# Performance work log

Measured on AMD Instinct MI355X. Metric: run time of the kernel, lower is better.

## Reference

```python
import jax, jax.numpy as jnp
import numpy as np

LAYER_SIZES = [128, 128, 64, 64, 64, 1]  # sMLP([128,128,64,64,64,1], 'relu')
B, DX, DY = 1024, 64, 64


def setup_inputs() -> dict:
    key = jax.random.key(0)
    ks = jax.random.split(key, 8)
    inp = {
        'x': jax.random.normal(ks[0], (B, DX), dtype=jnp.float32),
        'y': jax.random.normal(ks[1], (B, DY), dtype=jnp.float32),
    }
    dims = [DX + DY] + LAYER_SIZES
    for i in range(len(LAYER_SIZES)):
        fan_in, fan_out = dims[i], dims[i + 1]
        scale = jnp.sqrt(2.0 / (fan_in + fan_out)).astype(jnp.float32)  # glorot-like
        inp[f'W{i}'] = jax.random.normal(ks[2 + i % 6], (fan_in, fan_out), dtype=jnp.float32) * scale
        inp[f'b{i}'] = jnp.zeros((fan_out,), dtype=jnp.float32)
    return inp


def _mlp(h, Ws, bs):
    n = len(Ws)
    for i in range(n):
        h = h @ Ws[i] + bs[i]
        if i < n - 1:  # relu on hidden layers, linear output
            h = jax.nn.relu(h)
    return h


def reference(x, y, W0, b0, W1, b1, W2, b2, W3, b3, W4, b4, W5, b5):
    Bn = x.shape[0]
    dx, dy = x.shape[1], y.shape[1]
    # all-pairs tile+concat: row (i*B + j) = concat(x[j], y[i])
    x_tiled = jnp.broadcast_to(x[None, :, :], (Bn, Bn, dx))
    y_tiled = jnp.broadcast_to(y[:, None, :], (Bn, Bn, dy))
    xy_pairs = jnp.concatenate([x_tiled, y_tiled], axis=2).reshape(Bn * Bn, dx + dy)
    scores = _mlp(xy_pairs, [W0, W1, W2, W3, W4, W5], [b0, b1, b2, b3, b4, b5])
    scores = scores.reshape(Bn, Bn).T  # final[p, q] = g(x[p], y[q])
    return scores
```

## Files before the change

### kernel.cpp

```cpp
#include <hip/hip_runtime.h>

#define NB 1024

typedef _Float16 f16x8 __attribute__((ext_vector_type(8)));
typedef float f32x4 __attribute__((ext_vector_type(4)));

union ABu { uint4 u; f16x8 v; _Float16 h[8]; };

__global__ void prep_ac(const float* __restrict__ x, const float* __restrict__ y,
                        const float* __restrict__ W0, const float* __restrict__ b0,
                        _Float16* __restrict__ Af, _Float16* __restrict__ Cf) {
    __shared__ float row[64];
    int b = blockIdx.x;
    int t = threadIdx.x;
    bool isC = b >= 1024;
    int r = isC ? b - 1024 : b;
    const float* src = isC ? y : x;
    if (t < 64) row[t] = src[r * 64 + t];
    __syncthreads();
    const float* w = W0 + (isC ? 64 * 128 : 0);
    float acc = isC ? b0[t] : 0.f;
#pragma unroll
    for (int k = 0; k < 64; k++) acc += row[k] * w[k * 128 + t];
    (isC ? Cf : Af)[r * 128 + t] = (_Float16)acc;
}

__global__ void prep_img(const float* __restrict__ W1, const float* __restrict__ W2,
                         const float* __restrict__ W3, const float* __restrict__ W4,
                         _Float16* __restrict__ img) {
    int i = blockIdx.x * 256 + threadIdx.x;
    float val;
    if (i < 16384) {
        int j = i & 7, cc = (i >> 3) & 15, gg = (i >> 7) & 3, ks = (i >> 9) & 3, ft = i >> 11;
        int k = 32 * ks + 8 * gg + j, n = 16 * ft + cc;
        val = W1[k * 128 + n];
    } else if (i < 24576) {
        int d = i - 16384;
        int j = d & 7, cc = (d >> 3) & 15, gg = (d >> 7) & 3, ks = (d >> 9) & 3, ft = d >> 11;
        int s = 32 * ks + 8 * gg + j;
        int H = s >> 6, sp = s & 63;
        int a = ((sp >> 5) & 1) | (((sp >> 2) & 1) << 1);
        int gs = (sp >> 3) & 3, rr = sp & 3;
        int fin = 64 * H + 16 * a + 4 * gs + rr, n = 16 * ft + cc;
        val = W2[fin * 64 + n];
    } else {
        int d = (i < 28672) ? i - 24576 : i - 28672;
        const float* W = (i < 28672) ? W3 : W4;
        int j = d & 7, cc = (d >> 3) & 15, gg = (d >> 7) & 3, ks = (d >> 9) & 1, ft = d >> 10;
        int s = 32 * ks + 8 * gg + j;
        int a = ((s >> 5) & 1) | (((s >> 2) & 1) << 1);
        int gs = (s >> 3) & 3, rr = s & 3;
        int fin = 16 * a + 4 * gs + rr, n = 16 * ft + cc;
        val = W[fin * 64 + n];
    }
    img[i] = (_Float16)val;
}

#define MFMA(a, b, d) (d) = __builtin_amdgcn_mfma_f32_16x16x32_f16((a), (b), (d), 0, 0, 0)

#define W2OFF 32768
#define W3OFF 49152
#define W4OFF 57344

__launch_bounds__(512, 4)
__global__ void critic_main(const _Float16* __restrict__ Af, const _Float16* __restrict__ Cf,
                            const _Float16* __restrict__ Wimg,
                            const float* __restrict__ b1, const float* __restrict__ b2,
                            const float* __restrict__ b3, const float* __restrict__ b4,
                            const float* __restrict__ W5, const float* __restrict__ b5,
                            float* __restrict__ out) {
    __shared__ _Float16 Wl[32768];
    int tid = threadIdx.x;

    {
        const uint4* src = (const uint4*)Wimg;
        uint4* dst = (uint4*)Wl;
#pragma unroll
        for (int r = 0; r < 8; r++) dst[r * 512 + tid] = src[r * 512 + tid];
    }
    __syncthreads();

    int w = tid >> 6, lane = tid & 63;
    int g = lane >> 4, c = lane & 15;
    int pw = (blockIdx.x >> 6) * 16 + w * 2;
    int qb = (blockIdx.x & 63) * 16;
    const char* WB = (const char*)Wl;
    int lo = lane * 16;

    ABu af[4][2];
#pragma unroll
    for (int ks = 0; ks < 4; ks++) {
        ABu cv; cv.u = *(const uint4*)&Cf[(qb + c) * 128 + ks * 32 + 8 * g];
#pragma unroll
        for (int pt = 0; pt < 2; pt++) {
            ABu av; av.u = *(const uint4*)&Af[(pw + pt) * 128 + ks * 32 + 8 * g];
            f16x8 s = av.v + cv.v;
            f16x8 z = {};
            af[ks][pt].v = __builtin_elementwise_max(s, z);
        }
    }

    ABu bh1[4][2];
#pragma unroll
    for (int ft = 0; ft < 8; ft++) {
        const int Hq = ft >> 2, a3 = ft & 3, ksp = a3 & 1, hi = a3 >> 1;
        f32x4 binit = *(const f32x4*)&b1[ft * 16 + 4 * g];
        f32x4 acc[2] = {binit, binit};
#pragma unroll
        for (int ks = 0; ks < 4; ks++) {
            ABu wf; wf.u = *(const uint4*)(WB + ft * 4096 + ks * 1024 + lo);
#pragma unroll
            for (int pt = 0; pt < 2; pt++) MFMA(wf.v, af[ks][pt].v, acc[pt]);
        }
#pragma unroll
        for (int pt = 0; pt < 2; pt++)
#pragma unroll
            for (int r = 0; r < 4; r++)
                bh1[Hq * 2 + ksp][pt].h[hi * 4 + r] = (_Float16)fmaxf(acc[pt][r], 0.f);
    }

    ABu bh2[2][2];
#pragma unroll
    for (int ft = 0; ft < 4; ft++) {
        const int ksp = ft & 1, hi = ft >> 1;
        f32x4 binit = *(const f32x4*)&b2[ft * 16 + 4 * g];
        f32x4 acc[2] = {binit, binit};
#pragma unroll
        for (int ks = 0; ks < 4; ks++) {
            ABu wf; wf.u = *(const uint4*)(WB + W2OFF + ft * 4096 + ks * 1024 + lo);
#pragma unroll
            for (int pt = 0; pt < 2; pt++) MFMA(wf.v, bh1[ks][pt].v, acc[pt]);
        }
#pragma unroll
        for (int pt = 0; pt < 2; pt++)
#pragma unroll
            for (int r = 0; r < 4; r++)
                bh2[ksp][pt].h[hi * 4 + r] = (_Float16)fmaxf(acc[pt][r], 0.f);
    }

    ABu bh3[2][2];
#pragma unroll
    for (int ft = 0; ft < 4; ft++) {
        const int ksp = ft & 1, hi = ft >> 1;
        f32x4 binit = *(const f32x4*)&b3[ft * 16 + 4 * g];
        f32x4 acc[2] = {binit, binit};
#pragma unroll
        for (int ks = 0; ks < 2; ks++) {
            ABu wf; wf.u = *(const uint4*)(WB + W3OFF + ft * 2048 + ks * 1024 + lo);
#pragma unroll
            for (int pt = 0; pt < 2; pt++) MFMA(wf.v, bh2[ks][pt].v, acc[pt]);
        }
#pragma unroll
        for (int pt = 0; pt < 2; pt++)
#pragma unroll
            for (int r = 0; r < 4; r++)
                bh3[ksp][pt].h[hi * 4 + r] = (_Float16)fmaxf(acc[pt][r], 0.f);
    }

    float s0 = 0.f, s1 = 0.f;
#pragma unroll
    for (int ft = 0; ft < 4; ft++) {
        f32x4 binit = *(const f32x4*)&b4[ft * 16 + 4 * g];
        f32x4 ww    = *(const f32x4*)&W5[ft * 16 + 4 * g];
        f32x4 acc[2] = {binit, binit};
#pragma unroll
        for (int ks = 0; ks < 2; ks++) {
            ABu wf; wf.u = *(const uint4*)(WB + W4OFF + ft * 2048 + ks * 1024 + lo);
#pragma unroll
            for (int pt = 0; pt < 2; pt++) MFMA(wf.v, bh3[ks][pt].v, acc[pt]);
        }
#pragma unroll
        for (int r = 0; r < 4; r++) {
            s0 += fmaxf(acc[0][r], 0.f) * ww[r];
            s1 += fmaxf(acc[1][r], 0.f) * ww[r];
        }
    }

    float b5s = b5[0];
    s0 += __shfl_xor(s0, 16); s0 += __shfl_xor(s0, 32);
    s1 += __shfl_xor(s1, 16); s1 += __shfl_xor(s1, 32);
    if (lane < 16) {
        out[(pw + 0) * NB + qb + c] = s0 + b5s;
        out[(pw + 1) * NB + qb + c] = s1 + b5s;
    }
}

extern "C" void kernel_launch(void* const* d_in, const int* in_sizes, int n_in,
                              void* d_out, int out_size, void* d_ws, size_t ws_size,
                              hipStream_t stream) {
    const float* x  = (const float*)d_in[0];
    const float* y  = (const float*)d_in[1];
    const float* W0 = (const float*)d_in[2];
    const float* b0 = (const float*)d_in[3];
    const float* W1 = (const float*)d_in[4];
    const float* b1 = (const float*)d_in[5];
    const float* W2 = (const float*)d_in[6];
    const float* b2 = (const float*)d_in[7];
    const float* W3 = (const float*)d_in[8];
    const float* b3 = (const float*)d_in[9];
    const float* W4 = (const float*)d_in[10];
    const float* b4 = (const float*)d_in[11];
    const float* W5 = (const float*)d_in[12];
    const float* b5 = (const float*)d_in[13];
    float* out = (float*)d_out;

    char* ws = (char*)d_ws;
    _Float16* Af   = (_Float16*)ws;
    _Float16* Cf   = (_Float16*)(ws + 262144);
    _Float16* Wimg = (_Float16*)(ws + 524288);

    prep_ac<<<2048, 128, 0, stream>>>(x, y, W0, b0, Af, Cf);
    prep_img<<<128, 256, 0, stream>>>(W1, W2, W3, W4, Wimg);
    critic_main<<<4096, 512, 0, stream>>>(Af, Cf, Wimg,
                                          b1, b2, b3, b4, W5, b5, out);
}
```

Measured before the change: 80.70 us.

## Process four p-rows per wave and pack fp16 conversions with cvt_pkrtz

Each wave now handles four p-rows instead of two. Every weight fragment loaded from LDS therefore feeds four MFMAs instead of two, and the grid halves to 2048 blocks, so the per-block cost of staging the 64KB weight image into LDS is paid half as often. Activation conversion to fp16 now uses packed round-toward-zero conversions, which take fewer instructions but round differently. The larger register footprint forces launch bounds down to 2 blocks per CU, which cuts occupancy.

```diff
diff --git a/kernel.cpp b/kernel.cpp
--- a/kernel.cpp
+++ b/kernel.cpp
@@ -5,7 +5,12 @@
 typedef _Float16 f16x8 __attribute__((ext_vector_type(8)));
 typedef float f32x4 __attribute__((ext_vector_type(4)));
 
-union ABu { uint4 u; f16x8 v; _Float16 h[8]; };
+union ABu { uint4 u; f16x8 v; _Float16 h[8]; unsigned int w[4]; };
+
+__device__ __forceinline__ unsigned int pkrtz(float a, float b) {
+    __fp16 r2 __attribute__((ext_vector_type(2))) = __builtin_amdgcn_cvt_pkrtz(a, b);
+    return __builtin_bit_cast(unsigned int, r2);
+}
 
 __global__ void prep_ac(const float* __restrict__ x, const float* __restrict__ y,
                         const float* __restrict__ W0, const float* __restrict__ b0,
@@ -62,7 +67,7 @@
 #define W3OFF 49152
 #define W4OFF 57344
 
-__launch_bounds__(512, 4)
+__launch_bounds__(512, 2)
 __global__ void critic_main(const _Float16* __restrict__ Af, const _Float16* __restrict__ Cf,
                             const _Float16* __restrict__ Wimg,
                             const float* __restrict__ b1, const float* __restrict__ b2,
@@ -82,17 +87,17 @@
 
     int w = tid >> 6, lane = tid & 63;
     int g = lane >> 4, c = lane & 15;
-    int pw = (blockIdx.x >> 6) * 16 + w * 2;
+    int pw = (blockIdx.x >> 6) * 32 + w * 4;
     int qb = (blockIdx.x & 63) * 16;
     const char* WB = (const char*)Wl;
     int lo = lane * 16;
 
-    ABu af[4][2];
+    ABu af[4][4];
 #pragma unroll
     for (int ks = 0; ks < 4; ks++) {
         ABu cv; cv.u = *(const uint4*)&Cf[(qb + c) * 128 + ks * 32 + 8 * g];
 #pragma unroll
-        for (int pt = 0; pt < 2; pt++) {
+        for (int pt = 0; pt < 4; pt++) {
             ABu av; av.u = *(const uint4*)&Af[(pw + pt) * 128 + ks * 32 + 8 * g];
             f16x8 s = av.v + cv.v;
             f16x8 z = {};
@@ -100,88 +105,100 @@
         }
     }
 
-    ABu bh1[4][2];
+    ABu bh1[4][4];
 #pragma unroll
     for (int ft = 0; ft < 8; ft++) {
         const int Hq = ft >> 2, a3 = ft & 3, ksp = a3 & 1, hi = a3 >> 1;
         f32x4 binit = *(const f32x4*)&b1[ft * 16 + 4 * g];
-        f32x4 acc[2] = {binit, binit};
+        f32x4 acc[4] = {binit, binit, binit, binit};
 #pragma unroll
         for (int ks = 0; ks < 4; ks++) {
             ABu wf; wf.u = *(const uint4*)(WB + ft * 4096 + ks * 1024 + lo);
 #pragma unroll
-            for (int pt = 0; pt < 2; pt++) MFMA(wf.v, af[ks][pt].v, acc[pt]);
-        }
-#pragma unroll
-        for (int pt = 0; pt < 2; pt++)
-#pragma unroll
-            for (int r = 0; r < 4; r++)
-                bh1[Hq * 2 + ksp][pt].h[hi * 4 + r] = (_Float16)fmaxf(acc[pt][r], 0.f);
-    }
-
-    ABu bh2[2][2];
+            for (int pt = 0; pt < 4; pt++) MFMA(wf.v, af[ks][pt].v, acc[pt]);
+        }
+#pragma unroll
+        for (int pt = 0; pt < 4; pt++) {
+            bh1[Hq * 2 + ksp][pt].w[hi * 2 + 0] =
+                pkrtz(fmaxf(acc[pt][0], 0.f), fmaxf(acc[pt][1], 0.f));
+            bh1[Hq * 2 + ksp][pt].w[hi * 2 + 1] =
+                pkrtz(fmaxf(acc[pt][2], 0.f), fmaxf(acc[pt][3], 0.f));
+        }
+    }
+
+    ABu bh2[2][4];
 #pragma unroll
     for (int ft = 0; ft < 4; ft++) {
         const int ksp = ft & 1, hi = ft >> 1;
         f32x4 binit = *(const f32x4*)&b2[ft * 16 + 4 * g];
-        f32x4 acc[2] = {binit, binit};
+        f32x4 acc[4] = {binit, binit, binit, binit};
 #pragma unroll
         for (int ks = 0; ks < 4; ks++) {
             ABu wf; wf.u = *(const uint4*)(WB + W2OFF + ft * 4096 + ks * 1024 + lo);
 #pragma unroll
-            for (int pt = 0; pt < 2; pt++) MFMA(wf.v, bh1[ks][pt].v, acc[pt]);
-        }
-#pragma unroll
-        for (int pt = 0; pt < 2; pt++)
-#pragma unroll
-            for (int r = 0; r < 4; r++)
-                bh2[ksp][pt].h[hi * 4 + r] = (_Float16)fmaxf(acc[pt][r], 0.f);
-    }
-
-    ABu bh3[2][2];
+            for (int pt = 0; pt < 4; pt++) MFMA(wf.v, bh1[ks][pt].v, acc[pt]);
+        }
+#pragma unroll
+        for (int pt = 0; pt < 4; pt++) {
+            bh2[ksp][pt].w[hi * 2 + 0] =
+                pkrtz(fmaxf(acc[pt][0], 0.f), fmaxf(acc[pt][1], 0.f));
+            bh2[ksp][pt].w[hi * 2 + 1] =
+                pkrtz(fmaxf(acc[pt][2], 0.f), fmaxf(acc[pt][3], 0.f));
+        }
+    }
+
+    ABu bh3[2][4];
 #pragma unroll
     for (int ft = 0; ft < 4; ft++) {
         const int ksp = ft & 1, hi = ft >> 1;
         f32x4 binit = *(const f32x4*)&b3[ft * 16 + 4 * g];
-        f32x4 acc[2] = {binit, binit};
+        f32x4 acc[4] = {binit, binit, binit, binit};
 #pragma unroll
         for (int ks = 0; ks < 2; ks++) {
             ABu wf; wf.u = *(const uint4*)(WB + W3OFF + ft * 2048 + ks * 1024 + lo);
 #pragma unroll
-            for (int pt = 0; pt < 2; pt++) MFMA(wf.v, bh2[ks][pt].v, acc[pt]);
-        }
-#pragma unroll
-        for (int pt = 0; pt < 2; pt++)
-#pragma unroll
-            for (int r = 0; r < 4; r++)
-                bh3[ksp][pt].h[hi * 4 + r] = (_Float16)fmaxf(acc[pt][r], 0.f);
-    }
-
-    float s0 = 0.f, s1 = 0.f;
+            for (int pt = 0; pt < 4; pt++) MFMA(wf.v, bh2[ks][pt].v, acc[pt]);
+        }
+#pragma unroll
+        for (int pt = 0; pt < 4; pt++) {
+            bh3[ksp][pt].w[hi * 2 + 0] =
+                pkrtz(fmaxf(acc[pt][0], 0.f), fmaxf(acc[pt][1], 0.f));
+            bh3[ksp][pt].w[hi * 2 + 1] =
+                pkrtz(fmaxf(acc[pt][2], 0.f), fmaxf(acc[pt][3], 0.f));
+        }
+    }
+
+    float s0 = 0.f, s1 = 0.f, s2 = 0.f, s3 = 0.f;
 #pragma unroll
     for (int ft = 0; ft < 4; ft++) {
         f32x4 binit = *(const f32x4*)&b4[ft * 16 + 4 * g];
         f32x4 ww    = *(const f32x4*)&W5[ft * 16 + 4 * g];
-        f32x4 acc[2] = {binit, binit};
+        f32x4 acc[4] = {binit, binit, binit, binit};
 #pragma unroll
         for (int ks = 0; ks < 2; ks++) {
             ABu wf; wf.u = *(const uint4*)(WB + W4OFF + ft * 2048 + ks * 1024 + lo);
 #pragma unroll
-            for (int pt = 0; pt < 2; pt++) MFMA(wf.v, bh3[ks][pt].v, acc[pt]);
+            for (int pt = 0; pt < 4; pt++) MFMA(wf.v, bh3[ks][pt].v, acc[pt]);
         }
 #pragma unroll
         for (int r = 0; r < 4; r++) {
             s0 += fmaxf(acc[0][r], 0.f) * ww[r];
             s1 += fmaxf(acc[1][r], 0.f) * ww[r];
+            s2 += fmaxf(acc[2][r], 0.f) * ww[r];
+            s3 += fmaxf(acc[3][r], 0.f) * ww[r];
         }
     }
 
     float b5s = b5[0];
     s0 += __shfl_xor(s0, 16); s0 += __shfl_xor(s0, 32);
     s1 += __shfl_xor(s1, 16); s1 += __shfl_xor(s1, 32);
+    s2 += __shfl_xor(s2, 16); s2 += __shfl_xor(s2, 32);
+    s3 += __shfl_xor(s3, 16); s3 += __shfl_xor(s3, 32);
     if (lane < 16) {
         out[(pw + 0) * NB + qb + c] = s0 + b5s;
         out[(pw + 1) * NB + qb + c] = s1 + b5s;
+        out[(pw + 2) * NB + qb + c] = s2 + b5s;
+        out[(pw + 3) * NB + qb + c] = s3 + b5s;
     }
 }
 
@@ -211,6 +228,6 @@
 
     prep_ac<<<2048, 128, 0, stream>>>(x, y, W0, b0, Af, Cf);
     prep_img<<<128, 256, 0, stream>>>(W1, W2, W3, W4, Wimg);
-    critic_main<<<4096, 512, 0, stream>>>(Af, Cf, Wimg,
+    critic_main<<<2048, 512, 0, stream>>>(Af, Cf, Wimg,
                                           b1, b2, b3, b4, W5, b5, out);
 }
```

Result: slower. 99.25 us (+23.0%).
